# Optimization experiments

Hardware: AMD Instinct MI355X
Metric: run time of the kernel (lower is better)

The kernel has to match this reference:

```python
import jax, jax.numpy as jnp
import numpy as np

BATCH, DIM = 8192, 1024  # batch of ODE states, state dimension (orig dim=100 scaled up)
ETA = 1.0                # self.eta
B_DECAY = 1.0            # self.B (linear decay coefficient)


def setup_inputs() -> dict:
    key = jax.random.key(0)
    k1, k2, k3, k4, k5 = jax.random.split(key, 5)
    return {
        "x":      jax.random.normal(k1, (BATCH, DIM), jnp.float32),
        "e_x":    jax.random.normal(k2, (BATCH, DIM), jnp.float32),
        "W":      jax.random.normal(k3, (BATCH, DIM), jnp.float32),
        "A":      jax.random.normal(k4, (DIM, DIM), jnpp := jnp.float32) / np.float32(np.sqrt(DIM)),
        "target": jax.random.normal(k5, (1, DIM), jnp.float32),
    }


def reference(x, e_x, W, A, target):
    # b_ast = diagonal of B_ast = diag(target^2 / (1 + target^2)); mm with a diag
    # matrix == elementwise multiply by its diagonal.  [1, D]
    b_ast = target ** 2 / (1.0 + target ** 2)
    # control: u = -eta * (W * (x + e_x - target)) @ B_ast              [B, D]
    u = -ETA * (W * ((x + e_x) - target)) * b_ast
    # saturating nonlinearity sigma(x) = x^2 / (1 + x^2)                [B, D]
    sig = x ** 2 / (1.0 + x ** 2)
    # dx = -B*x + A @ sigma(x) (per state: sigma(x) @ A^T) + u*sigma(x) [B, D]
    dx = -B_DECAY * x + sig @ A.T + u * sig
    # original returns tuple(dx_i) + tuple(-dx_i) + tuple(zeros): stack as [3, B, D]
    return jnp.stack([dx, -dx, jnp.zeros_like(dx)])
```

## Files before the change

### kernel.cpp

```cpp
#include <hip/hip_runtime.h>
#include <hip/hip_bf16.h>
#include <stdint.h>

#define BATCH 8192
#define DIM   1024

typedef __attribute__((ext_vector_type(4))) float f32x4;
typedef __attribute__((ext_vector_type(8))) short bf16x8;
typedef __attribute__((ext_vector_type(4))) unsigned short u16x4;

#define AS1(p) ((const __attribute__((address_space(1))) void*)(p))
#define AS3(p) ((__attribute__((address_space(3))) void*)(p))

__device__ __forceinline__ unsigned short f2bf(float f) {
    union { float f; unsigned int u; } v; v.f = f;
    unsigned int u = v.u;
    u += 0x7fffu + ((u >> 16) & 1u);
    return (unsigned short)(u >> 16);
}

__global__ __launch_bounds__(256) void prep_kernel(
    const float* __restrict__ x, const float* __restrict__ ex,
    const float* __restrict__ W, const float* __restrict__ tgt,
    float* __restrict__ out0, float* __restrict__ out2,
    unsigned short* __restrict__ sigb)
{
    int idx  = blockIdx.x * 256 + threadIdx.x;
    int col4 = idx & (DIM / 4 - 1);

    f32x4 xv = ((const f32x4*)x)[idx];
    f32x4 ev = ((const f32x4*)ex)[idx];
    f32x4 wv = ((const f32x4*)W)[idx];
    f32x4 tv = ((const f32x4*)tgt)[col4];

    f32x4 base;
    u16x4 sb;
#pragma unroll
    for (int i = 0; i < 4; ++i) {
        float xi = xv[i], ti = tv[i];
        float b_ast = ti * ti / (1.0f + ti * ti);
        float u = -(wv[i] * (xi + ev[i] - ti)) * b_ast;
        float s = xi * xi / (1.0f + xi * xi);
        base[i] = -xi + u * s;
        sb[i] = f2bf(s);
    }
    ((f32x4*)out0)[idx] = base;
    ((f32x4*)out2)[idx] = f32x4{0.f, 0.f, 0.f, 0.f};
    ((u16x4*)sigb)[idx] = sb;
}

__global__ __launch_bounds__(256) void convA_kernel(
    const float* __restrict__ A, unsigned short* __restrict__ Ab)
{
    int idx = blockIdx.x * 256 + threadIdx.x;
    f32x4 av = ((const f32x4*)A)[idx];
    u16x4 ab;
#pragma unroll
    for (int i = 0; i < 4; ++i) ab[i] = f2bf(av[i]);
    ((u16x4*)Ab)[idx] = ab;
}

#define BM 128
#define BN 128
#define BK 64

__global__ __launch_bounds__(256) void gemm_kernel(
    const unsigned short* __restrict__ Sg,
    const unsigned short* __restrict__ Ab,
    float* __restrict__ out0, float* __restrict__ out1)
{
    __shared__ char lds[(BM * BK + BN * BK) * 2];
    char* As = lds;
    char* Bs = lds + BM * BK * 2;

    const int nbn = DIM / BN;
    const int bm = blockIdx.x / nbn;
    const int bn = blockIdx.x % nbn;

    const int tid  = threadIdx.x;
    const int lane = tid & 63;
    const int wid  = tid >> 6;
    const int wr   = wid >> 1;
    const int wc   = wid & 1;

    const int swz = (((lane & 7) ^ (lane >> 3)) << 4);
    const char* gA = (const char*)Sg +
        ((size_t)(bm * BM + wid * 32 + (lane >> 3)) * DIM) * 2 + swz;
    const char* gB = (const char*)Ab +
        ((size_t)(bn * BN + wid * 32 + (lane >> 3)) * DIM) * 2 + swz;
    char* lA = As + wid * 4 * 1024;
    char* lB = Bs + wid * 4 * 1024;

    const int arow  = wr * 64 + (lane & 15);
    const int brow  = wc * 64 + (lane & 15);
    const int rd_sw = (lane & 7) << 4;
    const int cb0   = (lane >> 4) << 4;

    f32x4 acc[4][4];
#pragma unroll
    for (int mi = 0; mi < 4; ++mi)
#pragma unroll
        for (int ni = 0; ni < 4; ++ni)
            acc[mi][ni] = f32x4{0.f, 0.f, 0.f, 0.f};

    for (int k0 = 0; k0 < DIM; k0 += BK) {
        __syncthreads();
#pragma unroll
        for (int j = 0; j < 4; ++j) {
            __builtin_amdgcn_global_load_lds(AS1(gA + (size_t)j * (8 * DIM * 2) + k0 * 2),
                                             AS3(lA + j * 1024), 16, 0, 0);
            __builtin_amdgcn_global_load_lds(AS1(gB + (size_t)j * (8 * DIM * 2) + k0 * 2),
                                             AS3(lB + j * 1024), 16, 0, 0);
        }
        __syncthreads();

#pragma unroll
        for (int kk = 0; kk < 2; ++kk) {
            bf16x8 af[4], bfr[4];
#pragma unroll
            for (int mi = 0; mi < 4; ++mi)
                af[mi] = *(const bf16x8*)(As + (arow + mi * 16) * 128 +
                                          ((cb0 + kk * 64) ^ rd_sw));
#pragma unroll
            for (int ni = 0; ni < 4; ++ni)
                bfr[ni] = *(const bf16x8*)(Bs + (brow + ni * 16) * 128 +
                                           ((cb0 + kk * 64) ^ rd_sw));
#pragma unroll
            for (int mi = 0; mi < 4; ++mi)
#pragma unroll
                for (int ni = 0; ni < 4; ++ni)
                    acc[mi][ni] = __builtin_amdgcn_mfma_f32_16x16x32_bf16(
                        af[mi], bfr[ni], acc[mi][ni], 0, 0, 0);
        }
    }

    const int col0  = bn * BN + wc * 64 + (lane & 15);
    const int row00 = bm * BM + wr * 64 + ((lane >> 4) << 2);
#pragma unroll
    for (int mi = 0; mi < 4; ++mi) {
#pragma unroll
        for (int ni = 0; ni < 4; ++ni) {
            const int col = col0 + ni * 16;
#pragma unroll
            for (int r = 0; r < 4; ++r) {
                size_t idx = (size_t)(row00 + mi * 16 + r) * DIM + col;
                float dx = out0[idx] + acc[mi][ni][r];
                out0[idx] = dx;
                out1[idx] = -dx;
            }
        }
    }
}

extern "C" void kernel_launch(void* const* d_in, const int* in_sizes, int n_in,
                              void* d_out, int out_size, void* d_ws, size_t ws_size,
                              hipStream_t stream)
{
    const float* x   = (const float*)d_in[0];
    const float* ex  = (const float*)d_in[1];
    const float* W   = (const float*)d_in[2];
    const float* A   = (const float*)d_in[3];
    const float* tgt = (const float*)d_in[4];

    float* out0 = (float*)d_out;
    float* out1 = out0 + (size_t)BATCH * DIM;
    float* out2 = out1 + (size_t)BATCH * DIM;

    unsigned short* sigb = (unsigned short*)d_ws;
    unsigned short* Abf  = (unsigned short*)((char*)d_ws + (size_t)BATCH * DIM * 2);

    prep_kernel<<<BATCH * DIM / 4 / 256, 256, 0, stream>>>(x, ex, W, tgt, out0, out2, sigb);
    convA_kernel<<<DIM * DIM / 4 / 256, 256, 0, stream>>>(A, Abf);
    gemm_kernel<<<(BATCH / BM) * (DIM / BN), 256, 0, stream>>>(sigb, Abf, out0, out1);
}
```

Baseline: 67.39 us.

## Fuse elementwise prep into GEMM: compute sigma on the fly and epilogue

Removes the separate prep kernel. The GEMM now reads x in fp32, computes sigma and converts it to bf16 directly into LDS for the A operand, and computes the u*sigma and -x terms in the epilogue from x, W, e_x and target. This avoids writing and re-reading the bf16 sigma buffer and the intermediate out0 round trip. In exchange, each N-tile block re-reads x in fp32 (8x redundancy across bn), the A operand loses the async global_load_lds path, and epilogue loads are strided scalar accesses. The change also adds an XCD-aware block remap and uses rcp in place of division.

```diff
diff --git a/kernel.cpp b/kernel.cpp
--- a/kernel.cpp
+++ b/kernel.cpp
@@ -4,10 +4,14 @@
 
 #define BATCH 8192
 #define DIM   1024
+#define BM 128
+#define BN 128
+#define BK 64
 
 typedef __attribute__((ext_vector_type(4))) float f32x4;
 typedef __attribute__((ext_vector_type(8))) short bf16x8;
 typedef __attribute__((ext_vector_type(4))) unsigned short u16x4;
+typedef __attribute__((ext_vector_type(8))) unsigned short u16x8;
 
 #define AS1(p) ((const __attribute__((address_space(1))) void*)(p))
 #define AS3(p) ((__attribute__((address_space(3))) void*)(p))
@@ -19,34 +23,9 @@
     return (unsigned short)(u >> 16);
 }
 
-__global__ __launch_bounds__(256) void prep_kernel(
-    const float* __restrict__ x, const float* __restrict__ ex,
-    const float* __restrict__ W, const float* __restrict__ tgt,
-    float* __restrict__ out0, float* __restrict__ out2,
-    unsigned short* __restrict__ sigb)
-{
-    int idx  = blockIdx.x * 256 + threadIdx.x;
-    int col4 = idx & (DIM / 4 - 1);
-
-    f32x4 xv = ((const f32x4*)x)[idx];
-    f32x4 ev = ((const f32x4*)ex)[idx];
-    f32x4 wv = ((const f32x4*)W)[idx];
-    f32x4 tv = ((const f32x4*)tgt)[col4];
-
-    f32x4 base;
-    u16x4 sb;
-#pragma unroll
-    for (int i = 0; i < 4; ++i) {
-        float xi = xv[i], ti = tv[i];
-        float b_ast = ti * ti / (1.0f + ti * ti);
-        float u = -(wv[i] * (xi + ev[i] - ti)) * b_ast;
-        float s = xi * xi / (1.0f + xi * xi);
-        base[i] = -xi + u * s;
-        sb[i] = f2bf(s);
-    }
-    ((f32x4*)out0)[idx] = base;
-    ((f32x4*)out2)[idx] = f32x4{0.f, 0.f, 0.f, 0.f};
-    ((u16x4*)sigb)[idx] = sb;
+__device__ __forceinline__ float sigma_f(float x) {
+    float x2 = x * x;
+    return x2 * __builtin_amdgcn_rcpf(1.0f + x2);
 }
 
 __global__ __launch_bounds__(256) void convA_kernel(
@@ -60,22 +39,22 @@
     ((u16x4*)Ab)[idx] = ab;
 }
 
-#define BM 128
-#define BN 128
-#define BK 64
-
-__global__ __launch_bounds__(256) void gemm_kernel(
-    const unsigned short* __restrict__ Sg,
+__global__ __launch_bounds__(256) void fused_kernel(
+    const float* __restrict__ x, const float* __restrict__ ex,
+    const float* __restrict__ W, const float* __restrict__ tgt,
     const unsigned short* __restrict__ Ab,
-    float* __restrict__ out0, float* __restrict__ out1)
+    float* __restrict__ out0, float* __restrict__ out1,
+    float* __restrict__ out2)
 {
-    __shared__ char lds[(BM * BK + BN * BK) * 2];
+    __shared__ char lds[(BM + BN) * BK * 2];
     char* As = lds;
     char* Bs = lds + BM * BK * 2;
 
-    const int nbn = DIM / BN;
-    const int bm = blockIdx.x / nbn;
-    const int bn = blockIdx.x % nbn;
+    const int p    = blockIdx.x;
+    const int xcd  = p & 7;
+    const int slot = p >> 3;
+    const int bm   = xcd * 8 + (slot >> 3);
+    const int bn   = slot & 7;
 
     const int tid  = threadIdx.x;
     const int lane = tid & 63;
@@ -84,12 +63,14 @@
     const int wc   = wid & 1;
 
     const int swz = (((lane & 7) ^ (lane >> 3)) << 4);
-    const char* gA = (const char*)Sg +
-        ((size_t)(bm * BM + wid * 32 + (lane >> 3)) * DIM) * 2 + swz;
     const char* gB = (const char*)Ab +
         ((size_t)(bn * BN + wid * 32 + (lane >> 3)) * DIM) * 2 + swz;
-    char* lA = As + wid * 4 * 1024;
     char* lB = Bs + wid * 4 * 1024;
+
+    const int r0 = tid >> 3;
+    const int g  = tid & 7;
+    const float* gx = x + (size_t)(bm * BM + r0) * DIM + g * 8;
+    char* wA = As + r0 * 128 + ((g * 16) ^ ((r0 & 7) << 4));
 
     const int arow  = wr * 64 + (lane & 15);
     const int brow  = wc * 64 + (lane & 15);
@@ -106,11 +87,20 @@
     for (int k0 = 0; k0 < DIM; k0 += BK) {
         __syncthreads();
 #pragma unroll
-        for (int j = 0; j < 4; ++j) {
-            __builtin_amdgcn_global_load_lds(AS1(gA + (size_t)j * (8 * DIM * 2) + k0 * 2),
-                                             AS3(lA + j * 1024), 16, 0, 0);
+        for (int j = 0; j < 4; ++j)
             __builtin_amdgcn_global_load_lds(AS1(gB + (size_t)j * (8 * DIM * 2) + k0 * 2),
                                              AS3(lB + j * 1024), 16, 0, 0);
+#pragma unroll
+        for (int j = 0; j < 4; ++j) {
+            f32x4 v0 = *(const f32x4*)(gx + (size_t)j * 32 * DIM + k0);
+            f32x4 v1 = *(const f32x4*)(gx + (size_t)j * 32 * DIM + k0 + 4);
+            u16x8 sb;
+#pragma unroll
+            for (int i = 0; i < 4; ++i) {
+                sb[i]     = f2bf(sigma_f(v0[i]));
+                sb[i + 4] = f2bf(sigma_f(v1[i]));
+            }
+            *(u16x8*)(wA + j * 32 * 128) = sb;
         }
         __syncthreads();
 
@@ -136,17 +126,32 @@
 
     const int col0  = bn * BN + wc * 64 + (lane & 15);
     const int row00 = bm * BM + wr * 64 + ((lane >> 4) << 2);
+
+    float b_ast[4];
+#pragma unroll
+    for (int ni = 0; ni < 4; ++ni) {
+        float t = tgt[col0 + ni * 16];
+        b_ast[ni] = t * t * __builtin_amdgcn_rcpf(1.0f + t * t);
+    }
+
 #pragma unroll
     for (int mi = 0; mi < 4; ++mi) {
 #pragma unroll
         for (int ni = 0; ni < 4; ++ni) {
             const int col = col0 + ni * 16;
+            const float t = tgt[col];
 #pragma unroll
             for (int r = 0; r < 4; ++r) {
                 size_t idx = (size_t)(row00 + mi * 16 + r) * DIM + col;
-                float dx = out0[idx] + acc[mi][ni][r];
+                float xi = x[idx];
+                float wi = W[idx];
+                float ei = ex[idx];
+                float u  = -(wi * (xi + ei - t)) * b_ast[ni];
+                float s  = sigma_f(xi);
+                float dx = -xi + u * s + acc[mi][ni][r];
                 out0[idx] = dx;
                 out1[idx] = -dx;
+                out2[idx] = 0.0f;
             }
         }
     }
@@ -166,10 +171,9 @@
     float* out1 = out0 + (size_t)BATCH * DIM;
     float* out2 = out1 + (size_t)BATCH * DIM;
 
-    unsigned short* sigb = (unsigned short*)d_ws;
-    unsigned short* Abf  = (unsigned short*)((char*)d_ws + (size_t)BATCH * DIM * 2);
+    unsigned short* Abf = (unsigned short*)d_ws;
 
-    prep_kernel<<<BATCH * DIM / 4 / 256, 256, 0, stream>>>(x, ex, W, tgt, out0, out2, sigb);
     convA_kernel<<<DIM * DIM / 4 / 256, 256, 0, stream>>>(A, Abf);
-    gemm_kernel<<<(BATCH / BM) * (DIM / BN), 256, 0, stream>>>(sigb, Abf, out0, out1);
+    fused_kernel<<<(BATCH / BM) * (DIM / BN), 256, 0, stream>>>(
+        x, ex, W, tgt, Abf, out0, out1, out2);
 }
```

New measurement: 70.35 us. 4.4% more time.
